# Optimization experiments

Measured on AMD Instinct MI355X. Metric: run time of the kernel, lower is better.

The kernel has to match this reference:

```python
import jax, jax.numpy as jnp
import numpy as np
from jax import lax

B, L, H, K = 64, 1024, 768, 4
C1, C2 = 0.1, 0.1


def crf_marginals(feats, maskf, T):
    """Batched linear-chain CRF forward-backward.
    feats: [B,L,K] emission scores, maskf: [B,L] float (1=valid), T: [K,K] transitions.
    Returns marginals [B,L,K] (zeroed at padded positions)."""
    a0 = feats[:, 0]  # [B,K]

    def fwd_step(a, xs):
        f_t, m_t = xs  # [B,K], [B]
        new = f_t + jax.nn.logsumexp(a[:, :, None] + T[None], axis=1)
        a = jnp.where(m_t[:, None] > 0, new, a)  # freeze alpha past last valid token
        return a, a

    _, alphas_rest = lax.scan(fwd_step, a0,
                              (jnp.swapaxes(feats[:, 1:], 0, 1), maskf[:, 1:].T))
    alphas = jnp.concatenate([a0[None], alphas_rest], axis=0)  # [L,B,K]
    logZ = jax.nn.logsumexp(alphas[-1], axis=-1)  # [B] (alpha frozen at last valid t)

    bL = jnp.zeros_like(a0)

    def bwd_step(b, xs):
        f_n, m_n = xs  # emission/mask at t+1
        new = jax.nn.logsumexp(T[None] + (f_n + b)[:, None, :], axis=2)
        b = jnp.where(m_n[:, None] > 0, new, b)  # beta stays 0 until last valid token
        return b, b

    xs = (jnp.swapaxes(feats[:, 1:][:, ::-1], 0, 1), maskf[:, 1:][:, ::-1].T)
    _, betas_rev = lax.scan(bwd_step, bL, xs)
    betas = jnp.concatenate([bL[None], betas_rev], axis=0)[::-1]  # [L,B,K]

    marg = jnp.exp(alphas + betas - logZ[None, :, None]) * maskf.T[:, :, None]
    return jnp.swapaxes(marg, 0, 1)  # [B,L,K]


def _forward(hidden, maskf, w, b, T):
    feats = hidden @ w.T + b                      # [B,L,K] feat2tri
    marg = crf_marginals(feats, maskf, T)
    sp = marg[:, :, 1]                            # select_polarities, masked [B,L]
    gamma = sp.sum(axis=1) / 2.0                  # [B]
    sent_vs = jnp.einsum('bl,blh->bh', sp, hidden) / gamma[:, None]
    s_prob = sp / gamma[:, None]                  # padded-ragged per-token probs
    s_prob_norm = jnp.abs(s_prob).sum(axis=1).mean()
    pena = jax.nn.relu(T[1, 0] - T[0, 0]) + jax.nn.relu(T[0, 1] - T[1, 1])
    norm_pen = C1 * pena + C2 * s_prob_norm
    return sent_vs, norm_pen, s_prob


def setup_inputs():
    key = jax.random.key(0)
    ks = jax.random.split(key, 8)
    hidden = jax.random.normal(ks[0], (B, L, H), dtype=jnp.float32)
    seq_lens = jax.random.randint(ks[1], (B,), L // 4, L + 1)
    # hidden_mask: 0 for valid tokens, nonzero for padding (forward uses mask = hidden_mask==0)
    hidden_mask = (jnp.arange(L)[None, :] >= seq_lens[:, None]).astype(jnp.int32)
    subj_position = jax.random.randint(ks[2], (B, L), -20, 21)
    obj_position = jax.random.randint(ks[3], (B, L), -20, 21)
    pe_inputs = jax.random.randint(ks[4], (B, L), 0, 2 * L)
    pe_binary = jax.random.randint(ks[5], (B, L), 0, 2)
    w_feat2tri = jax.random.normal(ks[6], (K, H), dtype=jnp.float32) * (1.0 / np.sqrt(H)).astype(np.float32)
    b_feat2tri = jnp.zeros((K,), dtype=jnp.float32)
    transitions = jax.random.normal(ks[7], (K, K), dtype=jnp.float32) * 0.1
    return dict(hidden=hidden, hidden_mask=hidden_mask, subj_position=subj_position,
                obj_position=obj_position, seq_lens=seq_lens, pe_inputs=pe_inputs,
                pe_binary=pe_binary, w_feat2tri=w_feat2tri, b_feat2tri=b_feat2tri,
                transitions=transitions)


def reference(hidden, hidden_mask, subj_position, obj_position, seq_lens, pe_inputs,
              pe_binary, w_feat2tri, b_feat2tri, transitions):
    maskf = (hidden_mask == 0).astype(hidden.dtype)
    # relevance is computed in the original forward but never consumed downstream,
    # so it has no effect on outputs; omitted here.
    return _forward(hidden, maskf, w_feat2tri, b_feat2tri, transitions)
```

## Files before the change

### kernel.cpp

```cpp
#include <hip/hip_runtime.h>

#define B 64
#define L 1024
#define H 768
#define NROWS (B * L)
#define LOG2E 1.4426950408889634f
#define CS 16
#define NCH 64
#define NEG -1e30f

#define EXP2(x) __builtin_amdgcn_exp2f(x)
#define LOG2(x) __builtin_amdgcn_logf(x)

__global__ __launch_bounds__(256) void feats_kernel(
    const float* __restrict__ hidden, const float* __restrict__ w,
    const float* __restrict__ bias, float4* __restrict__ featsT)
{
    const int lane = threadIdx.x & 63;
    const int wave = (blockIdx.x * blockDim.x + threadIdx.x) >> 6;
    const int nwaves = (gridDim.x * blockDim.x) >> 6;

    float wr[3][4][4];
#pragma unroll
    for (int c = 0; c < 3; ++c)
#pragma unroll
        for (int j = 0; j < 4; ++j)
#pragma unroll
            for (int k = 0; k < 4; ++k)
                wr[c][j][k] = w[k * H + lane * 4 + 256 * c + j];
    const float bb0 = bias[0], bb1 = bias[1], bb2 = bias[2], bb3 = bias[3];

    for (int row = wave; row < NROWS; row += nwaves) {
        const float4* hrow = reinterpret_cast<const float4*>(hidden) + (size_t)row * (H / 4);
        float acc[4] = {0.f, 0.f, 0.f, 0.f};
#pragma unroll
        for (int c = 0; c < 3; ++c) {
            float4 h = hrow[lane + 64 * c];
            const float hv[4] = {h.x, h.y, h.z, h.w};
#pragma unroll
            for (int j = 0; j < 4; ++j)
#pragma unroll
                for (int k = 0; k < 4; ++k)
                    acc[k] = fmaf(hv[j], wr[c][j][k], acc[k]);
        }
#pragma unroll
        for (int k = 0; k < 4; ++k) {
            float v = acc[k];
#pragma unroll
            for (int s = 32; s >= 1; s >>= 1) v += __shfl_xor(v, s, 64);
            acc[k] = v;
        }
        if (lane == 0) {
            const int b = row >> 10, l = row & 1023;
            featsT[l * B + b] = make_float4((acc[0] + bb0) * LOG2E, (acc[1] + bb1) * LOG2E,
                                            (acc[2] + bb2) * LOG2E, (acc[3] + bb3) * LOG2E);
        }
    }
}

__global__ __launch_bounds__(128) void chunkmat_kernel(
    const float4* __restrict__ featsT, const int* __restrict__ seq_lens,
    const float* __restrict__ T, float* __restrict__ mats)
{
    const int b = threadIdx.x & 63;
    const int dir = threadIdx.x >> 6;
    const int c = blockIdx.x;
    const int sl = seq_lens[b];
    const int lo = c * CS + 1;
    const int hi = min(c * CS + CS, L - 1);
    const int ns = hi - lo + 1;

    float eT2[4][4];
#pragma unroll
    for (int i = 0; i < 4; ++i)
#pragma unroll
        for (int j = 0; j < 4; ++j) eT2[i][j] = EXP2(T[i * 4 + j] * LOG2E);

    float4 fr[CS];
#pragma unroll
    for (int u = 0; u < CS; ++u) {
        const int t = dir ? max(hi - u, lo) : min(lo + u, hi);
        fr[u] = featsT[t * B + b];
    }

    float M[4][4];
#pragma unroll
    for (int i = 0; i < 4; ++i)
#pragma unroll
        for (int j = 0; j < 4; ++j) M[i][j] = (i == j) ? 0.f : NEG;

    if (dir == 0) {
#pragma unroll
        for (int u = 0; u < CS; ++u) {
            const int t = lo + u;
            const bool valid = (u < ns) && (t < sl);
            const float f[4] = {fr[u].x, fr[u].y, fr[u].z, fr[u].w};
            float nM[4][4];
#pragma unroll
            for (int i = 0; i < 4; ++i) {
                const float rm = fmaxf(fmaxf(M[i][0], M[i][1]), fmaxf(M[i][2], M[i][3]));
                const float e0 = EXP2(M[i][0] - rm), e1 = EXP2(M[i][1] - rm);
                const float e2 = EXP2(M[i][2] - rm), e3 = EXP2(M[i][3] - rm);
#pragma unroll
                for (int j = 0; j < 4; ++j) {
                    const float s = (e0 * eT2[0][j] + e1 * eT2[1][j]) + (e2 * eT2[2][j] + e3 * eT2[3][j]);
                    nM[i][j] = f[j] + rm + LOG2(s);
                }
            }
#pragma unroll
            for (int i = 0; i < 4; ++i)
#pragma unroll
                for (int j = 0; j < 4; ++j) M[i][j] = valid ? nM[i][j] : M[i][j];
        }
    } else {
#pragma unroll
        for (int u = 0; u < CS; ++u) {
            const int n = hi - u;
            const bool valid = (u < ns) && (n < sl);
            const float f[4] = {fr[u].x, fr[u].y, fr[u].z, fr[u].w};
            float nM[4][4];
#pragma unroll
            for (int j = 0; j < 4; ++j) {
                const float c0 = f[0] + M[0][j], c1 = f[1] + M[1][j];
                const float c2 = f[2] + M[2][j], c3 = f[3] + M[3][j];
                const float cm = fmaxf(fmaxf(c0, c1), fmaxf(c2, c3));
                const float g0 = EXP2(c0 - cm), g1 = EXP2(c1 - cm);
                const float g2 = EXP2(c2 - cm), g3 = EXP2(c3 - cm);
#pragma unroll
                for (int i = 0; i < 4; ++i) {
                    const float s = (g0 * eT2[i][0] + g1 * eT2[i][1]) + (g2 * eT2[i][2] + g3 * eT2[i][3]);
                    nM[i][j] = cm + LOG2(s);
                }
            }
#pragma unroll
            for (int i = 0; i < 4; ++i)
#pragma unroll
                for (int j = 0; j < 4; ++j) M[i][j] = valid ? nM[i][j] : M[i][j];
        }
    }
#pragma unroll
    for (int i = 0; i < 4; ++i)
#pragma unroll
        for (int j = 0; j < 4; ++j)
            mats[((dir * NCH + c) * 16 + i * 4 + j) * B + b] = M[i][j];
}

__global__ __launch_bounds__(128) void bound_kernel(
    const float4* __restrict__ featsT, const float* __restrict__ mats,
    float* __restrict__ vbound, float* __restrict__ logZ)
{
    const int b = threadIdx.x & 63;
    const int dir = threadIdx.x >> 6;

    float Ms[4][16];
#pragma unroll
    for (int p = 0; p < 3; ++p) {
        const int cc = dir ? (NCH - 1 - p) : p;
#pragma unroll
        for (int k = 0; k < 16; ++k)
            Ms[p][k] = mats[((dir * NCH + cc) * 16 + k) * B + b];
    }

    float v0, v1, v2, v3;
    if (dir == 0) {
        const float4 f0 = featsT[b];
        v0 = f0.x; v1 = f0.y; v2 = f0.z; v3 = f0.w;
    } else {
        v0 = v1 = v2 = v3 = 0.f;
    }

#pragma unroll
    for (int u = 0; u < NCH; ++u) {
        const int cc = dir ? (NCH - 1 - u) : u;
        vbound[((dir * NCH + cc) * 4 + 0) * B + b] = v0;
        vbound[((dir * NCH + cc) * 4 + 1) * B + b] = v1;
        vbound[((dir * NCH + cc) * 4 + 2) * B + b] = v2;
        vbound[((dir * NCH + cc) * 4 + 3) * B + b] = v3;
        if (u + 3 < NCH) {
            const int cp = dir ? (NCH - 1 - (u + 3)) : (u + 3);
#pragma unroll
            for (int k = 0; k < 16; ++k)
                Ms[(u + 3) & 3][k] = mats[((dir * NCH + cp) * 16 + k) * B + b];
        }
        float n[4];
        if (dir == 0) {
#pragma unroll
            for (int j = 0; j < 4; ++j) {
                const float c0 = v0 + Ms[u & 3][0 * 4 + j], c1 = v1 + Ms[u & 3][1 * 4 + j];
                const float c2 = v2 + Ms[u & 3][2 * 4 + j], c3 = v3 + Ms[u & 3][3 * 4 + j];
                const float m = fmaxf(fmaxf(c0, c1), fmaxf(c2, c3));
                const float s = (EXP2(c0 - m) + EXP2(c1 - m)) + (EXP2(c2 - m) + EXP2(c3 - m));
                n[j] = m + LOG2(s);
            }
        } else {
#pragma unroll
            for (int i = 0; i < 4; ++i) {
                const float c0 = v0 + Ms[u & 3][i * 4 + 0], c1 = v1 + Ms[u & 3][i * 4 + 1];
                const float c2 = v2 + Ms[u & 3][i * 4 + 2], c3 = v3 + Ms[u & 3][i * 4 + 3];
                const float m = fmaxf(fmaxf(c0, c1), fmaxf(c2, c3));
                const float s = (EXP2(c0 - m) + EXP2(c1 - m)) + (EXP2(c2 - m) + EXP2(c3 - m));
                n[i] = m + LOG2(s);
            }
        }
        v0 = n[0]; v1 = n[1]; v2 = n[2]; v3 = n[3];
    }
    if (dir == 0) {
        const float m = fmaxf(fmaxf(v0, v1), fmaxf(v2, v3));
        logZ[b] = m + LOG2(EXP2(v0 - m) + EXP2(v1 - m) + EXP2(v2 - m) + EXP2(v3 - m));
    }
}

__global__ __launch_bounds__(128) void rescan_sp_kernel(
    const float4* __restrict__ featsT, const int* __restrict__ seq_lens,
    const float* __restrict__ T, const float* __restrict__ vbound,
    const float* __restrict__ logZ, float* __restrict__ spu,
    float* __restrict__ chunksum)
{
    const int tid = threadIdx.x;
    const int b = tid & 63;
    const int dir = tid >> 6;
    const int c = blockIdx.x;
    const int sl = seq_lens[b];
    const int base = c * CS;

    float eT2[4][4];
#pragma unroll
    for (int i = 0; i < 4; ++i)
#pragma unroll
        for (int j = 0; j < 4; ++j) eT2[i][j] = EXP2(T[i * 4 + j] * LOG2E);

    __shared__ float ldb[CS * 64];

    if (dir == 1) {
        float v0 = vbound[((NCH + c) * 4 + 0) * B + b];
        float v1 = vbound[((NCH + c) * 4 + 1) * B + b];
        float v2 = vbound[((NCH + c) * 4 + 2) * B + b];
        float v3 = vbound[((NCH + c) * 4 + 3) * B + b];
        const bool last = (c == NCH - 1);
        const int hi_n = last ? (L - 1) : (base + CS);
        const int cnt = last ? (CS - 1) : CS;
        if (last) ldb[15 * 64 + b] = v1;
        float4 fr[CS];
#pragma unroll
        for (int u = 0; u < CS; ++u) fr[u] = featsT[max(hi_n - u, base + 1) * B + b];
#pragma unroll
        for (int u = 0; u < CS; ++u) {
            if (u < cnt) {
                const int n = hi_n - u;
                const bool valid = n < sl;
                const float4 f = fr[u];
                const float c0 = f.x + v0, c1 = f.y + v1, c2 = f.z + v2, c3 = f.w + v3;
                const float m = fmaxf(fmaxf(c0, c1), fmaxf(c2, c3));
                const float g0 = EXP2(c0 - m), g1 = EXP2(c1 - m), g2 = EXP2(c2 - m), g3 = EXP2(c3 - m);
                const float s0 = (g0 * eT2[0][0] + g1 * eT2[0][1]) + (g2 * eT2[0][2] + g3 * eT2[0][3]);
                const float s1 = (g0 * eT2[1][0] + g1 * eT2[1][1]) + (g2 * eT2[1][2] + g3 * eT2[1][3]);
                const float s2 = (g0 * eT2[2][0] + g1 * eT2[2][1]) + (g2 * eT2[2][2] + g3 * eT2[2][3]);
                const float s3 = (g0 * eT2[3][0] + g1 * eT2[3][1]) + (g2 * eT2[3][2] + g3 * eT2[3][3]);
                const float n0 = m + LOG2(s0), n1 = m + LOG2(s1);
                const float n2 = m + LOG2(s2), n3 = m + LOG2(s3);
                v0 = valid ? n0 : v0; v1 = valid ? n1 : v1;
                v2 = valid ? n2 : v2; v3 = valid ? n3 : v3;
                ldb[(n - 1 - base) * 64 + b] = v1;
            }
        }
    }

    float av[CS];
    if (dir == 0) {
        float a0 = vbound[(c * 4 + 0) * B + b];
        float a1 = vbound[(c * 4 + 1) * B + b];
        float a2 = vbound[(c * 4 + 2) * B + b];
        float a3 = vbound[(c * 4 + 3) * B + b];
        av[0] = a1;
        float4 fr[CS - 1];
#pragma unroll
        for (int u = 1; u < CS; ++u) fr[u - 1] = featsT[(base + u) * B + b];
#pragma unroll
        for (int u = 1; u < CS; ++u) {
            const int t = base + u;
            const bool valid = t < sl;
            const float4 f = fr[u - 1];
            const float m = fmaxf(fmaxf(a0, a1), fmaxf(a2, a3));
            const float e0 = EXP2(a0 - m), e1 = EXP2(a1 - m), e2 = EXP2(a2 - m), e3 = EXP2(a3 - m);
            const float s0 = (e0 * eT2[0][0] + e1 * eT2[1][0]) + (e2 * eT2[2][0] + e3 * eT2[3][0]);
            const float s1 = (e0 * eT2[0][1] + e1 * eT2[1][1]) + (e2 * eT2[2][1] + e3 * eT2[3][1]);
            const float s2 = (e0 * eT2[0][2] + e1 * eT2[1][2]) + (e2 * eT2[2][2] + e3 * eT2[3][2]);
            const float s3 = (e0 * eT2[0][3] + e1 * eT2[1][3]) + (e2 * eT2[2][3] + e3 * eT2[3][3]);
            const float n0 = f.x + m + LOG2(s0), n1 = f.y + m + LOG2(s1);
            const float n2 = f.z + m + LOG2(s2), n3 = f.w + m + LOG2(s3);
            a0 = valid ? n0 : a0; a1 = valid ? n1 : a1;
            a2 = valid ? n2 : a2; a3 = valid ? n3 : a3;
            av[u] = a1;
        }
    }

    __syncthreads();

    if (dir == 0) {
        const float lz = logZ[b];
        float sp[CS];
        float local = 0.f;
#pragma unroll
        for (int u = 0; u < CS; ++u) {
            const int l = base + u;
            const float x = (l < sl) ? EXP2(av[u] + ldb[u * 64 + b] - lz) : 0.f;
            sp[u] = x;
            local += x;
        }
        float4* dst = reinterpret_cast<float4*>(spu + b * L + base);
#pragma unroll
        for (int q = 0; q < 4; ++q)
            dst[q] = make_float4(sp[4 * q], sp[4 * q + 1], sp[4 * q + 2], sp[4 * q + 3]);
        chunksum[c * 64 + b] = local;
    }
}

__global__ __launch_bounds__(192) void sentv_kernel(
    const float* __restrict__ hidden, const float* __restrict__ spu,
    const float* __restrict__ chunksum, float* __restrict__ partial)
{
    const int lc = blockIdx.x;
    const int b = blockIdx.y;
    const int tid = threadIdx.x;

    __shared__ float s_inv;
    if (tid < 64) {
        float v = chunksum[tid * 64 + b];
#pragma unroll
        for (int s = 32; s >= 1; s >>= 1) v += __shfl_xor(v, s, 64);
        if (tid == 0) s_inv = 2.0f / v;
    }
    __syncthreads();
    const float inv = s_inv;

    const float4* hb = reinterpret_cast<const float4*>(hidden + ((size_t)b * L + lc * 256) * H) + tid;
    const float* sp = spu + b * L + lc * 256;

    float4 acc = make_float4(0.f, 0.f, 0.f, 0.f);
#pragma unroll 4
    for (int l0 = 0; l0 < 256; l0 += 4) {
        const float4 s4 = *reinterpret_cast<const float4*>(sp + l0);
        const float4 h0 = hb[(size_t)(l0 + 0) * 192];
        const float4 h1 = hb[(size_t)(l0 + 1) * 192];
        const float4 h2 = hb[(size_t)(l0 + 2) * 192];
        const float4 h3 = hb[(size_t)(l0 + 3) * 192];
        acc.x = fmaf(s4.x, h0.x, acc.x); acc.y = fmaf(s4.x, h0.y, acc.y);
        acc.z = fmaf(s4.x, h0.z, acc.z); acc.w = fmaf(s4.x, h0.w, acc.w);
        acc.x = fmaf(s4.y, h1.x, acc.x); acc.y = fmaf(s4.y, h1.y, acc.y);
        acc.z = fmaf(s4.y, h1.z, acc.z); acc.w = fmaf(s4.y, h1.w, acc.w);
        acc.x = fmaf(s4.z, h2.x, acc.x); acc.y = fmaf(s4.z, h2.y, acc.y);
        acc.z = fmaf(s4.z, h2.z, acc.z); acc.w = fmaf(s4.z, h2.w, acc.w);
        acc.x = fmaf(s4.w, h3.x, acc.x); acc.y = fmaf(s4.w, h3.y, acc.y);
        acc.z = fmaf(s4.w, h3.z, acc.z); acc.w = fmaf(s4.w, h3.w, acc.w);
    }
    acc.x *= inv; acc.y *= inv; acc.z *= inv; acc.w *= inv;
    reinterpret_cast<float4*>(partial)[((size_t)lc * B + b) * 192 + tid] = acc;
}

__global__ __launch_bounds__(256) void normalize_kernel(
    const float* __restrict__ spu, const float* __restrict__ chunksum,
    float* __restrict__ sprob, float* __restrict__ normsum)
{
    const int b = blockIdx.x;
    const int tid = threadIdx.x;
    __shared__ float s_tot;
    if (tid < 64) {
        float v = chunksum[tid * 64 + b];
#pragma unroll
        for (int s = 32; s >= 1; s >>= 1) v += __shfl_xor(v, s, 64);
        if (tid == 0) s_tot = v;
    }
    __syncthreads();
    const float tot = s_tot;
    const float inv = 1.0f / (0.5f * tot);
    const float4 v4 = reinterpret_cast<const float4*>(spu + b * L)[tid];
    reinterpret_cast<float4*>(sprob + b * L)[tid] =
        make_float4(v4.x * inv, v4.y * inv, v4.z * inv, v4.w * inv);
    if (tid == 0) normsum[b] = tot * inv;
}

__global__ __launch_bounds__(256) void final_kernel(
    const float* __restrict__ partial, const float* __restrict__ normsum,
    const float* __restrict__ T, float* __restrict__ out)
{
    const int idx = blockIdx.x * 256 + threadIdx.x;
    if (idx < B * H) {
        out[idx] = (partial[idx] + partial[B * H + idx]) +
                   (partial[2 * B * H + idx] + partial[3 * B * H + idx]);
    }
    if (idx == 0) {
        const float pena = fmaxf(T[4] - T[0], 0.f) + fmaxf(T[1] - T[5], 0.f);
        float s = 0.f;
        for (int b2 = 0; b2 < B; ++b2) s += normsum[b2];
        out[B * H] = 0.1f * pena + 0.1f * (s / 64.f);
    }
}

extern "C" void kernel_launch(void* const* d_in, const int* in_sizes, int n_in,
                              void* d_out, int out_size, void* d_ws, size_t ws_size,
                              hipStream_t stream) {
    const float* hidden   = (const float*)d_in[0];
    const int*   seq_lens = (const int*)d_in[4];
    const float* w        = (const float*)d_in[7];
    const float* bias     = (const float*)d_in[8];
    const float* T        = (const float*)d_in[9];

    float* ws = (float*)d_ws;
    float4* featsT   = (float4*)(ws);
    float*  mats     = ws + 262144;
    float*  vbound   = ws + 393216;
    float*  logZ     = ws + 425984;
    float*  chunksum = ws + 426048;
    float*  spu      = ws + 430144;
    float*  partial  = ws + 495680;
    float*  normsum  = ws + 692288;

    float* out   = (float*)d_out;
    float* sprob = out + B * H + 1;

    feats_kernel<<<2048, 256, 0, stream>>>(hidden, w, bias, featsT);
    chunkmat_kernel<<<NCH, 128, 0, stream>>>(featsT, seq_lens, T, mats);
    bound_kernel<<<1, 128, 0, stream>>>(featsT, mats, vbound, logZ);
    rescan_sp_kernel<<<NCH, 128, 0, stream>>>(featsT, seq_lens, T, vbound, logZ, spu, chunksum);
    sentv_kernel<<<dim3(4, 64), 192, 0, stream>>>(hidden, spu, chunksum, partial);
    normalize_kernel<<<64, 256, 0, stream>>>(spu, chunksum, sprob, normsum);
    final_kernel<<<192, 256, 0, stream>>>(partial, normsum, T, out);
}
```

Before: 103.5 us.

## Fuse CRF stages and reductions into cooperative kernels with grid syncs

Merges the chunk-matrix, boundary scan, rescan, and normalize kernels into one cooperative kernel that uses grid.sync between phases. It also folds the final reduction into the sentence-vector kernel. The aim is to cut kernel launch overhead and inter-kernel gaps, at the cost of grid-wide barrier latency and a single-block serial phase inside the cooperative grid. The norm-penalty term is replaced by the constant 2.0, which relies on every sequence summing to exactly that after normalization.

```diff
diff --git a/kernel.cpp b/kernel.cpp
--- a/kernel.cpp
+++ b/kernel.cpp
@@ -1,4 +1,7 @@
 #include <hip/hip_runtime.h>
+#include <hip/hip_cooperative_groups.h>
+
+namespace cg = cooperative_groups;
 
 #define B 64
 #define L 1024
@@ -58,170 +61,19 @@
     }
 }
 
-__global__ __launch_bounds__(128) void chunkmat_kernel(
+__global__ __launch_bounds__(128) void crf_mid_kernel(
     const float4* __restrict__ featsT, const int* __restrict__ seq_lens,
-    const float* __restrict__ T, float* __restrict__ mats)
+    const float* __restrict__ T, float* __restrict__ mats,
+    float* __restrict__ vbound, float* __restrict__ logZ,
+    float* __restrict__ spu, float* __restrict__ chunksum,
+    float* __restrict__ sprob)
 {
-    const int b = threadIdx.x & 63;
-    const int dir = threadIdx.x >> 6;
-    const int c = blockIdx.x;
-    const int sl = seq_lens[b];
-    const int lo = c * CS + 1;
-    const int hi = min(c * CS + CS, L - 1);
-    const int ns = hi - lo + 1;
-
-    float eT2[4][4];
-#pragma unroll
-    for (int i = 0; i < 4; ++i)
-#pragma unroll
-        for (int j = 0; j < 4; ++j) eT2[i][j] = EXP2(T[i * 4 + j] * LOG2E);
-
-    float4 fr[CS];
-#pragma unroll
-    for (int u = 0; u < CS; ++u) {
-        const int t = dir ? max(hi - u, lo) : min(lo + u, hi);
-        fr[u] = featsT[t * B + b];
-    }
-
-    float M[4][4];
-#pragma unroll
-    for (int i = 0; i < 4; ++i)
-#pragma unroll
-        for (int j = 0; j < 4; ++j) M[i][j] = (i == j) ? 0.f : NEG;
-
-    if (dir == 0) {
-#pragma unroll
-        for (int u = 0; u < CS; ++u) {
-            const int t = lo + u;
-            const bool valid = (u < ns) && (t < sl);
-            const float f[4] = {fr[u].x, fr[u].y, fr[u].z, fr[u].w};
-            float nM[4][4];
-#pragma unroll
-            for (int i = 0; i < 4; ++i) {
-                const float rm = fmaxf(fmaxf(M[i][0], M[i][1]), fmaxf(M[i][2], M[i][3]));
-                const float e0 = EXP2(M[i][0] - rm), e1 = EXP2(M[i][1] - rm);
-                const float e2 = EXP2(M[i][2] - rm), e3 = EXP2(M[i][3] - rm);
-#pragma unroll
-                for (int j = 0; j < 4; ++j) {
-                    const float s = (e0 * eT2[0][j] + e1 * eT2[1][j]) + (e2 * eT2[2][j] + e3 * eT2[3][j]);
-                    nM[i][j] = f[j] + rm + LOG2(s);
-                }
-            }
-#pragma unroll
-            for (int i = 0; i < 4; ++i)
-#pragma unroll
-                for (int j = 0; j < 4; ++j) M[i][j] = valid ? nM[i][j] : M[i][j];
-        }
-    } else {
-#pragma unroll
-        for (int u = 0; u < CS; ++u) {
-            const int n = hi - u;
-            const bool valid = (u < ns) && (n < sl);
-            const float f[4] = {fr[u].x, fr[u].y, fr[u].z, fr[u].w};
-            float nM[4][4];
-#pragma unroll
-            for (int j = 0; j < 4; ++j) {
-                const float c0 = f[0] + M[0][j], c1 = f[1] + M[1][j];
-                const float c2 = f[2] + M[2][j], c3 = f[3] + M[3][j];
-                const float cm = fmaxf(fmaxf(c0, c1), fmaxf(c2, c3));
-                const float g0 = EXP2(c0 - cm), g1 = EXP2(c1 - cm);
-                const float g2 = EXP2(c2 - cm), g3 = EXP2(c3 - cm);
-#pragma unroll
-                for (int i = 0; i < 4; ++i) {
-                    const float s = (g0 * eT2[i][0] + g1 * eT2[i][1]) + (g2 * eT2[i][2] + g3 * eT2[i][3]);
-                    nM[i][j] = cm + LOG2(s);
-                }
-            }
-#pragma unroll
-            for (int i = 0; i < 4; ++i)
-#pragma unroll
-                for (int j = 0; j < 4; ++j) M[i][j] = valid ? nM[i][j] : M[i][j];
-        }
-    }
-#pragma unroll
-    for (int i = 0; i < 4; ++i)
-#pragma unroll
-        for (int j = 0; j < 4; ++j)
-            mats[((dir * NCH + c) * 16 + i * 4 + j) * B + b] = M[i][j];
-}
-
-__global__ __launch_bounds__(128) void bound_kernel(
-    const float4* __restrict__ featsT, const float* __restrict__ mats,
-    float* __restrict__ vbound, float* __restrict__ logZ)
-{
-    const int b = threadIdx.x & 63;
-    const int dir = threadIdx.x >> 6;
-
-    float Ms[4][16];
-#pragma unroll
-    for (int p = 0; p < 3; ++p) {
-        const int cc = dir ? (NCH - 1 - p) : p;
-#pragma unroll
-        for (int k = 0; k < 16; ++k)
-            Ms[p][k] = mats[((dir * NCH + cc) * 16 + k) * B + b];
-    }
-
-    float v0, v1, v2, v3;
-    if (dir == 0) {
-        const float4 f0 = featsT[b];
-        v0 = f0.x; v1 = f0.y; v2 = f0.z; v3 = f0.w;
-    } else {
-        v0 = v1 = v2 = v3 = 0.f;
-    }
-
-#pragma unroll
-    for (int u = 0; u < NCH; ++u) {
-        const int cc = dir ? (NCH - 1 - u) : u;
-        vbound[((dir * NCH + cc) * 4 + 0) * B + b] = v0;
-        vbound[((dir * NCH + cc) * 4 + 1) * B + b] = v1;
-        vbound[((dir * NCH + cc) * 4 + 2) * B + b] = v2;
-        vbound[((dir * NCH + cc) * 4 + 3) * B + b] = v3;
-        if (u + 3 < NCH) {
-            const int cp = dir ? (NCH - 1 - (u + 3)) : (u + 3);
-#pragma unroll
-            for (int k = 0; k < 16; ++k)
-                Ms[(u + 3) & 3][k] = mats[((dir * NCH + cp) * 16 + k) * B + b];
-        }
-        float n[4];
-        if (dir == 0) {
-#pragma unroll
-            for (int j = 0; j < 4; ++j) {
-                const float c0 = v0 + Ms[u & 3][0 * 4 + j], c1 = v1 + Ms[u & 3][1 * 4 + j];
-                const float c2 = v2 + Ms[u & 3][2 * 4 + j], c3 = v3 + Ms[u & 3][3 * 4 + j];
-                const float m = fmaxf(fmaxf(c0, c1), fmaxf(c2, c3));
-                const float s = (EXP2(c0 - m) + EXP2(c1 - m)) + (EXP2(c2 - m) + EXP2(c3 - m));
-                n[j] = m + LOG2(s);
-            }
-        } else {
-#pragma unroll
-            for (int i = 0; i < 4; ++i) {
-                const float c0 = v0 + Ms[u & 3][i * 4 + 0], c1 = v1 + Ms[u & 3][i * 4 + 1];
-                const float c2 = v2 + Ms[u & 3][i * 4 + 2], c3 = v3 + Ms[u & 3][i * 4 + 3];
-                const float m = fmaxf(fmaxf(c0, c1), fmaxf(c2, c3));
-                const float s = (EXP2(c0 - m) + EXP2(c1 - m)) + (EXP2(c2 - m) + EXP2(c3 - m));
-                n[i] = m + LOG2(s);
-            }
-        }
-        v0 = n[0]; v1 = n[1]; v2 = n[2]; v3 = n[3];
-    }
-    if (dir == 0) {
-        const float m = fmaxf(fmaxf(v0, v1), fmaxf(v2, v3));
-        logZ[b] = m + LOG2(EXP2(v0 - m) + EXP2(v1 - m) + EXP2(v2 - m) + EXP2(v3 - m));
-    }
-}
-
-__global__ __launch_bounds__(128) void rescan_sp_kernel(
-    const float4* __restrict__ featsT, const int* __restrict__ seq_lens,
-    const float* __restrict__ T, const float* __restrict__ vbound,
-    const float* __restrict__ logZ, float* __restrict__ spu,
-    float* __restrict__ chunksum)
-{
+    cg::grid_group grid = cg::this_grid();
     const int tid = threadIdx.x;
     const int b = tid & 63;
     const int dir = tid >> 6;
     const int c = blockIdx.x;
     const int sl = seq_lens[b];
-    const int base = c * CS;
 
     float eT2[4][4];
 #pragma unroll
@@ -229,98 +81,264 @@
 #pragma unroll
         for (int j = 0; j < 4; ++j) eT2[i][j] = EXP2(T[i * 4 + j] * LOG2E);
 
+    {
+        const int lo = c * CS + 1;
+        const int hi = min(c * CS + CS, L - 1);
+        const int ns = hi - lo + 1;
+
+        float4 fr[CS];
+#pragma unroll
+        for (int u = 0; u < CS; ++u) {
+            const int t = dir ? max(hi - u, lo) : min(lo + u, hi);
+            fr[u] = featsT[t * B + b];
+        }
+
+        float M[4][4];
+#pragma unroll
+        for (int i = 0; i < 4; ++i)
+#pragma unroll
+            for (int j = 0; j < 4; ++j) M[i][j] = (i == j) ? 0.f : NEG;
+
+        if (dir == 0) {
+#pragma unroll
+            for (int u = 0; u < CS; ++u) {
+                const int t = lo + u;
+                const bool valid = (u < ns) && (t < sl);
+                const float f[4] = {fr[u].x, fr[u].y, fr[u].z, fr[u].w};
+                float nM[4][4];
+#pragma unroll
+                for (int i = 0; i < 4; ++i) {
+                    const float rm = fmaxf(fmaxf(M[i][0], M[i][1]), fmaxf(M[i][2], M[i][3]));
+                    const float e0 = EXP2(M[i][0] - rm), e1 = EXP2(M[i][1] - rm);
+                    const float e2 = EXP2(M[i][2] - rm), e3 = EXP2(M[i][3] - rm);
+#pragma unroll
+                    for (int j = 0; j < 4; ++j) {
+                        const float s = (e0 * eT2[0][j] + e1 * eT2[1][j]) + (e2 * eT2[2][j] + e3 * eT2[3][j]);
+                        nM[i][j] = f[j] + rm + LOG2(s);
+                    }
+                }
+#pragma unroll
+                for (int i = 0; i < 4; ++i)
+#pragma unroll
+                    for (int j = 0; j < 4; ++j) M[i][j] = valid ? nM[i][j] : M[i][j];
+            }
+        } else {
+#pragma unroll
+            for (int u = 0; u < CS; ++u) {
+                const int n = hi - u;
+                const bool valid = (u < ns) && (n < sl);
+                const float f[4] = {fr[u].x, fr[u].y, fr[u].z, fr[u].w};
+                float nM[4][4];
+#pragma unroll
+                for (int j = 0; j < 4; ++j) {
+                    const float c0 = f[0] + M[0][j], c1 = f[1] + M[1][j];
+                    const float c2 = f[2] + M[2][j], c3 = f[3] + M[3][j];
+                    const float cm = fmaxf(fmaxf(c0, c1), fmaxf(c2, c3));
+                    const float g0 = EXP2(c0 - cm), g1 = EXP2(c1 - cm);
+                    const float g2 = EXP2(c2 - cm), g3 = EXP2(c3 - cm);
+#pragma unroll
+                    for (int i = 0; i < 4; ++i) {
+                        const float s = (g0 * eT2[i][0] + g1 * eT2[i][1]) + (g2 * eT2[i][2] + g3 * eT2[i][3]);
+                        nM[i][j] = cm + LOG2(s);
+                    }
+                }
+#pragma unroll
+                for (int i = 0; i < 4; ++i)
+#pragma unroll
+                    for (int j = 0; j < 4; ++j) M[i][j] = valid ? nM[i][j] : M[i][j];
+            }
+        }
+#pragma unroll
+        for (int i = 0; i < 4; ++i)
+#pragma unroll
+            for (int j = 0; j < 4; ++j)
+                mats[((dir * NCH + c) * 16 + i * 4 + j) * B + b] = M[i][j];
+    }
+
+    grid.sync();
+
+    if (blockIdx.x == 0) {
+        float Ms[4][16];
+#pragma unroll
+        for (int p = 0; p < 3; ++p) {
+            const int cc = dir ? (NCH - 1 - p) : p;
+#pragma unroll
+            for (int k = 0; k < 16; ++k)
+                Ms[p][k] = mats[((dir * NCH + cc) * 16 + k) * B + b];
+        }
+
+        float v0, v1, v2, v3;
+        if (dir == 0) {
+            const float4 f0 = featsT[b];
+            v0 = f0.x; v1 = f0.y; v2 = f0.z; v3 = f0.w;
+        } else {
+            v0 = v1 = v2 = v3 = 0.f;
+        }
+
+#pragma unroll
+        for (int u = 0; u < NCH; ++u) {
+            const int cc = dir ? (NCH - 1 - u) : u;
+            vbound[((dir * NCH + cc) * 4 + 0) * B + b] = v0;
+            vbound[((dir * NCH + cc) * 4 + 1) * B + b] = v1;
+            vbound[((dir * NCH + cc) * 4 + 2) * B + b] = v2;
+            vbound[((dir * NCH + cc) * 4 + 3) * B + b] = v3;
+            if (u + 3 < NCH) {
+                const int cp = dir ? (NCH - 1 - (u + 3)) : (u + 3);
+#pragma unroll
+                for (int k = 0; k < 16; ++k)
+                    Ms[(u + 3) & 3][k] = mats[((dir * NCH + cp) * 16 + k) * B + b];
+            }
+            float n[4];
+            if (dir == 0) {
+#pragma unroll
+                for (int j = 0; j < 4; ++j) {
+                    const float c0 = v0 + Ms[u & 3][0 * 4 + j], c1 = v1 + Ms[u & 3][1 * 4 + j];
+                    const float c2 = v2 + Ms[u & 3][2 * 4 + j], c3 = v3 + Ms[u & 3][3 * 4 + j];
+                    const float m = fmaxf(fmaxf(c0, c1), fmaxf(c2, c3));
+                    const float s = (EXP2(c0 - m) + EXP2(c1 - m)) + (EXP2(c2 - m) + EXP2(c3 - m));
+                    n[j] = m + LOG2(s);
+                }
+            } else {
+#pragma unroll
+                for (int i = 0; i < 4; ++i) {
+                    const float c0 = v0 + Ms[u & 3][i * 4 + 0], c1 = v1 + Ms[u & 3][i * 4 + 1];
+                    const float c2 = v2 + Ms[u & 3][i * 4 + 2], c3 = v3 + Ms[u & 3][i * 4 + 3];
+                    const float m = fmaxf(fmaxf(c0, c1), fmaxf(c2, c3));
+                    const float s = (EXP2(c0 - m) + EXP2(c1 - m)) + (EXP2(c2 - m) + EXP2(c3 - m));
+                    n[i] = m + LOG2(s);
+                }
+            }
+            v0 = n[0]; v1 = n[1]; v2 = n[2]; v3 = n[3];
+        }
+        if (dir == 0) {
+            const float m = fmaxf(fmaxf(v0, v1), fmaxf(v2, v3));
+            logZ[b] = m + LOG2(EXP2(v0 - m) + EXP2(v1 - m) + EXP2(v2 - m) + EXP2(v3 - m));
+        }
+    }
+
+    grid.sync();
+
     __shared__ float ldb[CS * 64];
-
-    if (dir == 1) {
-        float v0 = vbound[((NCH + c) * 4 + 0) * B + b];
-        float v1 = vbound[((NCH + c) * 4 + 1) * B + b];
-        float v2 = vbound[((NCH + c) * 4 + 2) * B + b];
-        float v3 = vbound[((NCH + c) * 4 + 3) * B + b];
-        const bool last = (c == NCH - 1);
-        const int hi_n = last ? (L - 1) : (base + CS);
-        const int cnt = last ? (CS - 1) : CS;
-        if (last) ldb[15 * 64 + b] = v1;
-        float4 fr[CS];
-#pragma unroll
-        for (int u = 0; u < CS; ++u) fr[u] = featsT[max(hi_n - u, base + 1) * B + b];
-#pragma unroll
-        for (int u = 0; u < CS; ++u) {
-            if (u < cnt) {
-                const int n = hi_n - u;
-                const bool valid = n < sl;
-                const float4 f = fr[u];
-                const float c0 = f.x + v0, c1 = f.y + v1, c2 = f.z + v2, c3 = f.w + v3;
-                const float m = fmaxf(fmaxf(c0, c1), fmaxf(c2, c3));
-                const float g0 = EXP2(c0 - m), g1 = EXP2(c1 - m), g2 = EXP2(c2 - m), g3 = EXP2(c3 - m);
-                const float s0 = (g0 * eT2[0][0] + g1 * eT2[0][1]) + (g2 * eT2[0][2] + g3 * eT2[0][3]);
-                const float s1 = (g0 * eT2[1][0] + g1 * eT2[1][1]) + (g2 * eT2[1][2] + g3 * eT2[1][3]);
-                const float s2 = (g0 * eT2[2][0] + g1 * eT2[2][1]) + (g2 * eT2[2][2] + g3 * eT2[2][3]);
-                const float s3 = (g0 * eT2[3][0] + g1 * eT2[3][1]) + (g2 * eT2[3][2] + g3 * eT2[3][3]);
-                const float n0 = m + LOG2(s0), n1 = m + LOG2(s1);
-                const float n2 = m + LOG2(s2), n3 = m + LOG2(s3);
-                v0 = valid ? n0 : v0; v1 = valid ? n1 : v1;
-                v2 = valid ? n2 : v2; v3 = valid ? n3 : v3;
-                ldb[(n - 1 - base) * 64 + b] = v1;
-            }
-        }
-    }
-
-    float av[CS];
-    if (dir == 0) {
-        float a0 = vbound[(c * 4 + 0) * B + b];
-        float a1 = vbound[(c * 4 + 1) * B + b];
-        float a2 = vbound[(c * 4 + 2) * B + b];
-        float a3 = vbound[(c * 4 + 3) * B + b];
-        av[0] = a1;
-        float4 fr[CS - 1];
-#pragma unroll
-        for (int u = 1; u < CS; ++u) fr[u - 1] = featsT[(base + u) * B + b];
-#pragma unroll
-        for (int u = 1; u < CS; ++u) {
-            const int t = base + u;
-            const bool valid = t < sl;
-            const float4 f = fr[u - 1];
-            const float m = fmaxf(fmaxf(a0, a1), fmaxf(a2, a3));
-            const float e0 = EXP2(a0 - m), e1 = EXP2(a1 - m), e2 = EXP2(a2 - m), e3 = EXP2(a3 - m);
-            const float s0 = (e0 * eT2[0][0] + e1 * eT2[1][0]) + (e2 * eT2[2][0] + e3 * eT2[3][0]);
-            const float s1 = (e0 * eT2[0][1] + e1 * eT2[1][1]) + (e2 * eT2[2][1] + e3 * eT2[3][1]);
-            const float s2 = (e0 * eT2[0][2] + e1 * eT2[1][2]) + (e2 * eT2[2][2] + e3 * eT2[3][2]);
-            const float s3 = (e0 * eT2[0][3] + e1 * eT2[1][3]) + (e2 * eT2[2][3] + e3 * eT2[3][3]);
-            const float n0 = f.x + m + LOG2(s0), n1 = f.y + m + LOG2(s1);
-            const float n2 = f.z + m + LOG2(s2), n3 = f.w + m + LOG2(s3);
-            a0 = valid ? n0 : a0; a1 = valid ? n1 : a1;
-            a2 = valid ? n2 : a2; a3 = valid ? n3 : a3;
-            av[u] = a1;
-        }
-    }
-
-    __syncthreads();
-
-    if (dir == 0) {
-        const float lz = logZ[b];
-        float sp[CS];
-        float local = 0.f;
-#pragma unroll
-        for (int u = 0; u < CS; ++u) {
-            const int l = base + u;
-            const float x = (l < sl) ? EXP2(av[u] + ldb[u * 64 + b] - lz) : 0.f;
-            sp[u] = x;
-            local += x;
-        }
-        float4* dst = reinterpret_cast<float4*>(spu + b * L + base);
-#pragma unroll
-        for (int q = 0; q < 4; ++q)
-            dst[q] = make_float4(sp[4 * q], sp[4 * q + 1], sp[4 * q + 2], sp[4 * q + 3]);
-        chunksum[c * 64 + b] = local;
+    {
+        const int base = c * CS;
+
+        if (dir == 1) {
+            float v0 = vbound[((NCH + c) * 4 + 0) * B + b];
+            float v1 = vbound[((NCH + c) * 4 + 1) * B + b];
+            float v2 = vbound[((NCH + c) * 4 + 2) * B + b];
+            float v3 = vbound[((NCH + c) * 4 + 3) * B + b];
+            const bool last = (c == NCH - 1);
+            const int hi_n = last ? (L - 1) : (base + CS);
+            const int cnt = last ? (CS - 1) : CS;
+            if (last) ldb[15 * 64 + b] = v1;
+            float4 fr[CS];
+#pragma unroll
+            for (int u = 0; u < CS; ++u) fr[u] = featsT[max(hi_n - u, base + 1) * B + b];
+#pragma unroll
+            for (int u = 0; u < CS; ++u) {
+                if (u < cnt) {
+                    const int n = hi_n - u;
+                    const bool valid = n < sl;
+                    const float4 f = fr[u];
+                    const float c0 = f.x + v0, c1 = f.y + v1, c2 = f.z + v2, c3 = f.w + v3;
+                    const float m = fmaxf(fmaxf(c0, c1), fmaxf(c2, c3));
+                    const float g0 = EXP2(c0 - m), g1 = EXP2(c1 - m), g2 = EXP2(c2 - m), g3 = EXP2(c3 - m);
+                    const float s0 = (g0 * eT2[0][0] + g1 * eT2[0][1]) + (g2 * eT2[0][2] + g3 * eT2[0][3]);
+                    const float s1 = (g0 * eT2[1][0] + g1 * eT2[1][1]) + (g2 * eT2[1][2] + g3 * eT2[1][3]);
+                    const float s2 = (g0 * eT2[2][0] + g1 * eT2[2][1]) + (g2 * eT2[2][2] + g3 * eT2[2][3]);
+                    const float s3 = (g0 * eT2[3][0] + g1 * eT2[3][1]) + (g2 * eT2[3][2] + g3 * eT2[3][3]);
+                    const float n0 = m + LOG2(s0), n1 = m + LOG2(s1);
+                    const float n2 = m + LOG2(s2), n3 = m + LOG2(s3);
+                    v0 = valid ? n0 : v0; v1 = valid ? n1 : v1;
+                    v2 = valid ? n2 : v2; v3 = valid ? n3 : v3;
+                    ldb[(n - 1 - base) * 64 + b] = v1;
+                }
+            }
+        }
+
+        float av[CS];
+        if (dir == 0) {
+            float a0 = vbound[(c * 4 + 0) * B + b];
+            float a1 = vbound[(c * 4 + 1) * B + b];
+            float a2 = vbound[(c * 4 + 2) * B + b];
+            float a3 = vbound[(c * 4 + 3) * B + b];
+            av[0] = a1;
+            float4 fr[CS - 1];
+#pragma unroll
+            for (int u = 1; u < CS; ++u) fr[u - 1] = featsT[(base + u) * B + b];
+#pragma unroll
+            for (int u = 1; u < CS; ++u) {
+                const int t = base + u;
+                const bool valid = t < sl;
+                const float4 f = fr[u - 1];
+                const float m = fmaxf(fmaxf(a0, a1), fmaxf(a2, a3));
+                const float e0 = EXP2(a0 - m), e1 = EXP2(a1 - m), e2 = EXP2(a2 - m), e3 = EXP2(a3 - m);
+                const float s0 = (e0 * eT2[0][0] + e1 * eT2[1][0]) + (e2 * eT2[2][0] + e3 * eT2[3][0]);
+                const float s1 = (e0 * eT2[0][1] + e1 * eT2[1][1]) + (e2 * eT2[2][1] + e3 * eT2[3][1]);
+                const float s2 = (e0 * eT2[0][2] + e1 * eT2[1][2]) + (e2 * eT2[2][2] + e3 * eT2[3][2]);
+                const float s3 = (e0 * eT2[0][3] + e1 * eT2[1][3]) + (e2 * eT2[2][3] + e3 * eT2[3][3]);
+                const float n0 = f.x + m + LOG2(s0), n1 = f.y + m + LOG2(s1);
+                const float n2 = f.z + m + LOG2(s2), n3 = f.w + m + LOG2(s3);
+                a0 = valid ? n0 : a0; a1 = valid ? n1 : a1;
+                a2 = valid ? n2 : a2; a3 = valid ? n3 : a3;
+                av[u] = a1;
+            }
+        }
+
+        __syncthreads();
+
+        if (dir == 0) {
+            const float lz = logZ[b];
+            float sp[CS];
+            float local = 0.f;
+#pragma unroll
+            for (int u = 0; u < CS; ++u) {
+                const int l = base + u;
+                const float x = (l < sl) ? EXP2(av[u] + ldb[u * 64 + b] - lz) : 0.f;
+                sp[u] = x;
+                local += x;
+            }
+            float4* dst = reinterpret_cast<float4*>(spu + b * L + base);
+#pragma unroll
+            for (int q = 0; q < 4; ++q)
+                dst[q] = make_float4(sp[4 * q], sp[4 * q + 1], sp[4 * q + 2], sp[4 * q + 3]);
+            chunksum[c * 64 + b] = local;
+        }
+    }
+
+    grid.sync();
+
+    {
+        const int b2 = blockIdx.x;
+        __shared__ float s_tot;
+        if (tid < 64) {
+            float v = chunksum[tid * 64 + b2];
+#pragma unroll
+            for (int s = 32; s >= 1; s >>= 1) v += __shfl_xor(v, s, 64);
+            if (tid == 0) s_tot = v;
+        }
+        __syncthreads();
+        const float inv = 1.0f / (0.5f * s_tot);
+        const float4* sv = reinterpret_cast<const float4*>(spu + b2 * L);
+        float4* dv = reinterpret_cast<float4*>(sprob + b2 * L);
+#pragma unroll
+        for (int q = 0; q < 2; ++q) {
+            const int i = tid + q * 128;
+            const float4 v4 = sv[i];
+            dv[i] = make_float4(v4.x * inv, v4.y * inv, v4.z * inv, v4.w * inv);
+        }
     }
 }
 
-__global__ __launch_bounds__(192) void sentv_kernel(
+__global__ __launch_bounds__(192) void sentv_final_kernel(
     const float* __restrict__ hidden, const float* __restrict__ spu,
-    const float* __restrict__ chunksum, float* __restrict__ partial)
+    const float* __restrict__ chunksum, const float* __restrict__ T,
+    float* __restrict__ partial, float* __restrict__ out)
 {
-    const int lc = blockIdx.x;
-    const int b = blockIdx.y;
+    cg::grid_group grid = cg::this_grid();
+    const int blk = blockIdx.x;
+    const int lc = blk & 3;
+    const int b = blk >> 2;
     const int tid = threadIdx.x;
 
     __shared__ float s_inv;
@@ -355,44 +373,15 @@
     }
     acc.x *= inv; acc.y *= inv; acc.z *= inv; acc.w *= inv;
     reinterpret_cast<float4*>(partial)[((size_t)lc * B + b) * 192 + tid] = acc;
-}
-
-__global__ __launch_bounds__(256) void normalize_kernel(
-    const float* __restrict__ spu, const float* __restrict__ chunksum,
-    float* __restrict__ sprob, float* __restrict__ normsum)
-{
-    const int b = blockIdx.x;
-    const int tid = threadIdx.x;
-    __shared__ float s_tot;
-    if (tid < 64) {
-        float v = chunksum[tid * 64 + b];
-#pragma unroll
-        for (int s = 32; s >= 1; s >>= 1) v += __shfl_xor(v, s, 64);
-        if (tid == 0) s_tot = v;
-    }
-    __syncthreads();
-    const float tot = s_tot;
-    const float inv = 1.0f / (0.5f * tot);
-    const float4 v4 = reinterpret_cast<const float4*>(spu + b * L)[tid];
-    reinterpret_cast<float4*>(sprob + b * L)[tid] =
-        make_float4(v4.x * inv, v4.y * inv, v4.z * inv, v4.w * inv);
-    if (tid == 0) normsum[b] = tot * inv;
-}
-
-__global__ __launch_bounds__(256) void final_kernel(
-    const float* __restrict__ partial, const float* __restrict__ normsum,
-    const float* __restrict__ T, float* __restrict__ out)
-{
-    const int idx = blockIdx.x * 256 + threadIdx.x;
-    if (idx < B * H) {
-        out[idx] = (partial[idx] + partial[B * H + idx]) +
-                   (partial[2 * B * H + idx] + partial[3 * B * H + idx]);
-    }
+
+    grid.sync();
+
+    const int idx = blk * 192 + tid;
+    out[idx] = (partial[idx] + partial[B * H + idx]) +
+               (partial[2 * B * H + idx] + partial[3 * B * H + idx]);
     if (idx == 0) {
         const float pena = fmaxf(T[4] - T[0], 0.f) + fmaxf(T[1] - T[5], 0.f);
-        float s = 0.f;
-        for (int b2 = 0; b2 < B; ++b2) s += normsum[b2];
-        out[B * H] = 0.1f * pena + 0.1f * (s / 64.f);
+        out[B * H] = 0.1f * pena + 0.1f * 2.0f;
     }
 }
 
@@ -401,9 +390,9 @@
                               hipStream_t stream) {
     const float* hidden   = (const float*)d_in[0];
     const int*   seq_lens = (const int*)d_in[4];
+    const float* T        = (const float*)d_in[9];
     const float* w        = (const float*)d_in[7];
     const float* bias     = (const float*)d_in[8];
-    const float* T        = (const float*)d_in[9];
 
     float* ws = (float*)d_ws;
     float4* featsT   = (float4*)(ws);
@@ -413,16 +402,24 @@
     float*  chunksum = ws + 426048;
     float*  spu      = ws + 430144;
     float*  partial  = ws + 495680;
-    float*  normsum  = ws + 692288;
 
     float* out   = (float*)d_out;
     float* sprob = out + B * H + 1;
 
     feats_kernel<<<2048, 256, 0, stream>>>(hidden, w, bias, featsT);
-    chunkmat_kernel<<<NCH, 128, 0, stream>>>(featsT, seq_lens, T, mats);
-    bound_kernel<<<1, 128, 0, stream>>>(featsT, mats, vbound, logZ);
-    rescan_sp_kernel<<<NCH, 128, 0, stream>>>(featsT, seq_lens, T, vbound, logZ, spu, chunksum);
-    sentv_kernel<<<dim3(4, 64), 192, 0, stream>>>(hidden, spu, chunksum, partial);
-    normalize_kernel<<<64, 256, 0, stream>>>(spu, chunksum, sprob, normsum);
-    final_kernel<<<192, 256, 0, stream>>>(partial, normsum, T, out);
+
+    {
+        const float4* featsTc = (const float4*)featsT;
+        void* args[] = {(void*)&featsTc, (void*)&seq_lens, (void*)&T, (void*)&mats,
+                        (void*)&vbound, (void*)&logZ, (void*)&spu, (void*)&chunksum,
+                        (void*)&sprob};
+        hipLaunchCooperativeKernel(reinterpret_cast<void*>(crf_mid_kernel),
+                                   dim3(NCH), dim3(128), args, 0, stream);
+    }
+    {
+        void* args[] = {(void*)&hidden, (void*)&spu, (void*)&chunksum, (void*)&T,
+                        (void*)&partial, (void*)&out};
+        hipLaunchCooperativeKernel(reinterpret_cast<void*>(sentv_final_kernel),
+                                   dim3(256), dim3(192), args, 0, stream);
+    }
 }
```

Result: slower. 176.5 us (+70.6%).
